# Kernel optimization log

Measured on AMD Instinct MI355X. Metric: run time of the kernel, lower is better.

Reference implementation:

```python
import jax, jax.numpy as jnp
import numpy as np

B, C_IN, H, W = 64, 2048, 14, 14
D, FF, G, NC, NH = 768, 2048, 100, 9605, 8
DF = int(NC / G + 0.999)  # 97
HD = D // NH
EPS = 1e-5


def _ln(x, g, b):
    m = jnp.mean(x, axis=-1, keepdims=True)
    v = jnp.mean(jnp.square(x - m), axis=-1, keepdims=True)
    return (x - m) * jax.lax.rsqrt(v + EPS) * g + b


def setup_inputs() -> dict:
    key = jax.random.key(0)
    ks = jax.random.split(key, 16)
    def xav(k, shape):
        fan_in, fan_out = shape[-1], shape[-2] if len(shape) > 1 else shape[-1]
        std = float(np.sqrt(2.0 / (fan_in + fan_out)))
        return jax.random.normal(k, shape, jnp.float32) * std
    return {
        "x": jax.random.normal(ks[0], (B, C_IN, H, W), jnp.float32),
        "w_embed": xav(ks[1], (D, C_IN)), "b_embed": jnp.zeros((D,), jnp.float32),
        "query_embed": jax.random.normal(ks[2], (G, D), jnp.float32),
        "wq": xav(ks[3], (D, D)), "bq": jnp.zeros((D,), jnp.float32),
        "wk": xav(ks[4], (D, D)), "bk": jnp.zeros((D,), jnp.float32),
        "wv": xav(ks[5], (D, D)), "bv": jnp.zeros((D,), jnp.float32),
        "wo": xav(ks[6], (D, D)), "bo": jnp.zeros((D,), jnp.float32),
        "g1": jnp.ones((D,), jnp.float32), "be1": jnp.zeros((D,), jnp.float32),
        "g2": jnp.ones((D,), jnp.float32), "be2": jnp.zeros((D,), jnp.float32),
        "g3": jnp.ones((D,), jnp.float32), "be3": jnp.zeros((D,), jnp.float32),
        "w1": xav(ks[7], (FF, D)), "bl1": jnp.zeros((FF,), jnp.float32),
        "w2": xav(ks[8], (D, FF)), "bl2": jnp.zeros((D,), jnp.float32),
        "dup_pool": xav(ks[9], (G, D, DF)),
        "dup_bias": jnp.zeros((NC,), jnp.float32),
    }


def reference(x, w_embed, b_embed, query_embed, wq, bq, wk, bk, wv, bv, wo, bo,
              g1, be1, g2, be2, g3, be3, w1, bl1, w2, bl2, dup_pool, dup_bias):
    bs = x.shape[0]
    # [B, C, H, W] -> [B, S, C]
    mem = x.reshape(bs, x.shape[1], -1).transpose(0, 2, 1)
    # embed_standart + relu -> [B, S, D]
    mem = jax.nn.relu(jnp.einsum('bsc,dc->bsd', mem, w_embed) + b_embed)
    # tgt = queries broadcast to batch: [B, G, D]
    tgt = jnp.broadcast_to(query_embed[None], (bs, G, D))
    # layer: tgt = norm1(tgt + dropout1(tgt)) = norm1(2*tgt)
    tgt = _ln(tgt + tgt, g1, be1)
    # cross multihead attention (q=tgt, k=v=mem)
    q = (jnp.einsum('bgd,ed->bge', tgt, wq) + bq).reshape(bs, G, NH, HD)
    k = (jnp.einsum('bsd,ed->bse', mem, wk) + bk).reshape(bs, -1, NH, HD)
    v = (jnp.einsum('bsd,ed->bse', mem, wv) + bv).reshape(bs, -1, NH, HD)
    scores = jnp.einsum('bghd,bshd->bhgs', q, k) / jnp.sqrt(jnp.float32(HD))
    attn = jax.nn.softmax(scores, axis=-1)
    ctx = jnp.einsum('bhgs,bshd->bghd', attn, v).reshape(bs, G, D)
    ctx = jnp.einsum('bgd,ed->bge', ctx, wo) + bo
    tgt = _ln(tgt + ctx, g2, be2)
    # FFN
    ff = jax.nn.relu(jnp.einsum('bgd,fd->bgf', tgt, w1) + bl1)
    ff = jnp.einsum('bgf,df->bgd', ff, w2) + bl2
    h = _ln(tgt + ff, g3, be3)  # [B, G, D]
    # grouped FC: per-group matmul fused into one batched einsum
    out_extrap = jnp.einsum('bgd,gdf->bgf', h, dup_pool)  # [B, G, DF]
    logits = out_extrap.reshape(bs, G * DF)[:, :NC] + dup_bias
    return logits
```

## Files before the change

kernel.cpp:

```cpp
#include <hip/hip_runtime.h>
#include <hip/hip_bf16.h>


#define B_    64
#define CIN_  2048
#define S_    196
#define D_    768
#define FF_   2048
#define G_    100
#define NC_   9605
#define NH_   8
#define HD_   96
#define DF_   97
#define FP_   112
#define GP_   112
#define SP_   224
#define BS_   (B_ * S_)
#define BG_   (B_ * G_)

typedef __bf16 bf16x8 __attribute__((ext_vector_type(8)));
typedef float  f32x4  __attribute__((ext_vector_type(4)));
typedef ushort us8    __attribute__((ext_vector_type(8)));

__device__ __forceinline__ float bf2f(ushort u) {
  union { unsigned int i; float f; } v; v.i = ((unsigned int)u) << 16; return v.f;
}
__device__ __forceinline__ ushort f2bf(float f) {
  __hip_bfloat16 h = __float2bfloat16(f);
  return *reinterpret_cast<ushort*>(&h);
}

__device__ __forceinline__ void gl2lds16(const ushort* g, ushort* l) {
  __builtin_amdgcn_global_load_lds((const __attribute__((address_space(1))) unsigned int*)g,
                                   (__attribute__((address_space(3))) unsigned int*)l, 16, 0, 0);
}

#define XP_BLKS  4096
#define CVP_BLKS 256
#define TG_BLKS  128

struct PrepArgs {
  const float* x;   ushort* aemb;
  const float* csrc[2]; ushort* cdst[2]; int cn4[2]; int ctotal;
  const float* qe; const float* g1; const float* be1;
  float* tgt; ushort* tgtB;
};

__global__ __launch_bounds__(256) void k_prep(PrepArgs pa) {
  __shared__ __align__(16) char smem[196 * 40 * 2];
  int jid = blockIdx.x;
  const int t = threadIdx.x;

  if (jid < XP_BLKS) {
    ushort* xs = (ushort*)smem;
    const int b = jid >> 6, cbase = (jid & 63) * 32;
    const float* xb = pa.x + ((size_t)b * CIN_ + cbase) * S_;
    #pragma unroll
    for (int it = 0; it < 2; ++it) {
      const int u = it * 256 + t;
      if (u < 392) {
        const int j = u >> 3, cq = u & 7;
        const int s = 4 * j;
        float4 a[4];
        #pragma unroll
        for (int r = 0; r < 4; ++r)
          a[r] = *(const float4*)(xb + (size_t)(cq * 4 + r) * S_ + s);
        #pragma unroll
        for (int r = 0; r < 4; ++r) {
          ushort4 o;
          o.x = f2bf(((const float*)&a[0])[r]);
          o.y = f2bf(((const float*)&a[1])[r]);
          o.z = f2bf(((const float*)&a[2])[r]);
          o.w = f2bf(((const float*)&a[3])[r]);
          *(ushort4*)&xs[(s + r) * 40 + cq * 4] = o;
        }
      }
    }
    __syncthreads();
    const int sl = t >> 2, oct = t & 3;
    #pragma unroll
    for (int sr = 0; sr < 4; ++sr) {
      const int s = sr * 64 + sl;
      if (s < S_) {
        us8 v = *(const us8*)&xs[s * 40 + oct * 8];
        *(us8*)&pa.aemb[((size_t)(b * S_ + s)) * CIN_ + cbase + oct * 8] = v;
      }
    }
    return;
  }
  jid -= XP_BLKS;

  if (jid < CVP_BLKS) {
    int i = jid * 256 + t;
    const int stride = CVP_BLKS * 256;
    for (; i < pa.ctotal; i += stride) {
      int seg = 0, off = i;
      while (off >= pa.cn4[seg]) { off -= pa.cn4[seg]; ++seg; }
      const float4* sp = (const float4*)pa.csrc[seg];
      float4 v0 = sp[2 * off], v1 = sp[2 * off + 1];
      us8 o;
      o[0] = f2bf(v0.x); o[1] = f2bf(v0.y); o[2] = f2bf(v0.z); o[3] = f2bf(v0.w);
      o[4] = f2bf(v1.x); o[5] = f2bf(v1.y); o[6] = f2bf(v1.z); o[7] = f2bf(v1.w);
      ((us8*)pa.cdst[seg])[off] = o;
    }
    return;
  }
  jid -= CVP_BLKS;

  float* r1 = (float*)smem;
  float* r2 = r1 + 256;
  const int g = jid;
  if (g >= G_) {
    for (int d = t; d < D_; d += 256) pa.tgtB[(size_t)g * D_ + d] = 0;
    return;
  }
  float y[3]; float s = 0.f, sq = 0.f;
  const float* row = pa.qe + (size_t)g * D_;
  #pragma unroll
  for (int i = 0; i < 3; ++i) { float v = 2.f * row[t + i * 256]; y[i] = v; s += v; sq += v * v; }
  r1[t] = s; r2[t] = sq; __syncthreads();
  for (int o = 128; o > 0; o >>= 1) { if (t < o) { r1[t] += r1[t + o]; r2[t] += r2[t + o]; } __syncthreads(); }
  const float mean = r1[0] * (1.f / D_);
  const float var  = r2[0] * (1.f / D_) - mean * mean;
  const float w = rsqrtf(var + 1e-5f);
  #pragma unroll
  for (int i = 0; i < 3; ++i) {
    int d = t + i * 256;
    float v = (y[i] - mean) * w * pa.g1[d] + pa.be1[d];
    pa.tgt[(size_t)g * D_ + d] = v;
    pa.tgtB[(size_t)g * D_ + d] = f2bf(v);
  }
}

__device__ __forceinline__ void gemm_core(const ushort* __restrict__ A, const ushort* __restrict__ B,
    const float* __restrict__ bias, const float* __restrict__ bias2,
    float* __restrict__ Cf, ushort* __restrict__ Cb, ushort* __restrict__ Vt,
    int N, int K, int m0, int n0, int relu, ushort* As, ushort* Bs) {
  const int t = threadIdx.x;
  const int lane = t & 63, wave = t >> 6;
  const int quad = lane >> 4, lrow = lane & 15;
  const int wr = (wave >> 1) * 64, wc = (wave & 1) * 64;
  const int srow = t >> 2, scol = (t & 3) * 8;
  const ushort* ag = A + (size_t)(m0 + srow) * K + scol;
  const ushort* bg = B + (size_t)(n0 + srow) * K + scol;
  ushort* asw = As + t * 8;
  ushort* bsw = Bs + t * 8;
  f32x4 acc[4][4] = {};
  gl2lds16(ag,                  asw);
  gl2lds16(ag + (size_t)64 * K, asw + 64 * 32);
  gl2lds16(bg,                  bsw);
  gl2lds16(bg + (size_t)64 * K, bsw + 64 * 32);
  int cur = 0;
  for (int k0 = 0; k0 < K; k0 += 32) {
    if (k0 + 32 < K) {
      const int nb = (cur ^ 1) * (128 * 32);
      gl2lds16(ag + k0 + 32,                  asw + nb);
      gl2lds16(ag + k0 + 32 + (size_t)64 * K, asw + nb + 64 * 32);
      gl2lds16(bg + k0 + 32,                  bsw + nb);
      gl2lds16(bg + k0 + 32 + (size_t)64 * K, bsw + nb + 64 * 32);
      asm volatile("s_waitcnt vmcnt(4)" ::: "memory");
    } else {
      asm volatile("s_waitcnt vmcnt(0)" ::: "memory");
    }
    __builtin_amdgcn_s_barrier();
    __builtin_amdgcn_sched_barrier(0);
    const ushort* as = As + cur * (128 * 32);
    const ushort* bs = Bs + cur * (128 * 32);
    bf16x8 af[4], bfr[4];
    #pragma unroll
    for (int i = 0; i < 4; ++i) af[i] = *(const bf16x8*)&as[(wr + i * 16 + lrow) * 32 + quad * 8];
    #pragma unroll
    for (int j = 0; j < 4; ++j) bfr[j] = *(const bf16x8*)&bs[(wc + j * 16 + lrow) * 32 + quad * 8];
    __builtin_amdgcn_s_setprio(1);
    #pragma unroll
    for (int i = 0; i < 4; ++i)
      #pragma unroll
      for (int j = 0; j < 4; ++j)
        acc[i][j] = __builtin_amdgcn_mfma_f32_16x16x32_bf16(af[i], bfr[j], acc[i][j], 0, 0, 0);
    __builtin_amdgcn_s_setprio(0);
    __builtin_amdgcn_sched_barrier(0);
    __builtin_amdgcn_s_barrier();
    __builtin_amdgcn_sched_barrier(0);
    cur ^= 1;
  }
  #pragma unroll
  for (int i = 0; i < 4; ++i) {
    #pragma unroll
    for (int j = 0; j < 4; ++j) {
      const int gcol = n0 + wc + j * 16 + lrow;
      const float bv = (bias2 && gcol >= D_) ? bias2[gcol - D_] : (bias ? bias[gcol] : 0.f);
      if (Vt && gcol >= D_) {
        const int dv = gcol - D_, hh = dv / HD_, hd = dv % HD_;
        const int row0 = m0 + wr + i * 16 + quad * 4;
        const int bb = row0 / S_, ss = row0 % S_;
        ushort4 o;
        o.x = f2bf(acc[i][j][0] + bv);
        o.y = f2bf(acc[i][j][1] + bv);
        o.z = f2bf(acc[i][j][2] + bv);
        o.w = f2bf(acc[i][j][3] + bv);
        *(ushort4*)&Vt[((size_t)(bb * NH_ + hh) * HD_ + hd) * SP_ + ss] = o;
      } else {
        #pragma unroll
        for (int r = 0; r < 4; ++r) {
          const int grow = m0 + wr + i * 16 + quad * 4 + r;
          float v = acc[i][j][r] + bv;
          if (relu) v = fmaxf(v, 0.f);
          if (Cf) Cf[(size_t)grow * N + gcol] = v;
          else    Cb[(size_t)grow * N + gcol] = f2bf(v);
        }
      }
    }
  }
}

__global__ __launch_bounds__(256) void k_gemm(const ushort* __restrict__ A, const ushort* __restrict__ B,
    const float* __restrict__ bias, const float* __restrict__ bias2,
    float* __restrict__ Cf, ushort* __restrict__ Cb, ushort* __restrict__ Vt,
    int N, int K, int nbx, int nm, int relu) {
  __shared__ ushort As[2 * 128 * 32];
  __shared__ ushort Bs[2 * 128 * 32];
  const int l = blockIdx.x;
  const int mb = (l >> 3) / nbx * 8 + (l & 7);
  const int nb = (l >> 3) % nbx;
  if (mb >= nm) return;
  gemm_core(A, B, bias, bias2, Cf, Cb, Vt, N, K, mb * 128, nb * 128, relu, As, Bs);
}
static inline int swz_grid(int nm, int nbx) { return ((nm + 7) & ~7) * nbx; }

__device__ __forceinline__ void gemm_core64(const ushort* __restrict__ A, const ushort* __restrict__ B,
    const float* __restrict__ bias, ushort* __restrict__ Cb,
    int N, int K, int m0, int n0, int relu, ushort* As, ushort* Bs) {
  const int t = threadIdx.x;
  const int lane = t & 63, wave = t >> 6;
  const int quad = lane >> 4, lrow = lane & 15;
  const int wr = (wave >> 1) * 32, wc = (wave & 1) * 64;
  const int srow = t >> 2, scol = (t & 3) * 8;
  const ushort* ag = A + (size_t)(m0 + srow) * K + scol;
  const ushort* bg = B + (size_t)(n0 + srow) * K + scol;
  ushort* asw = As + t * 8;
  ushort* bsw = Bs + t * 8;
  f32x4 acc[2][4] = {};
  gl2lds16(ag,                  asw);
  gl2lds16(bg,                  bsw);
  gl2lds16(bg + (size_t)64 * K, bsw + 64 * 32);
  int cur = 0;
  for (int k0 = 0; k0 < K; k0 += 32) {
    if (k0 + 32 < K) {
      gl2lds16(ag + k0 + 32,                  asw + (cur ^ 1) * (64 * 32));
      gl2lds16(bg + k0 + 32,                  bsw + (cur ^ 1) * (128 * 32));
      gl2lds16(bg + k0 + 32 + (size_t)64 * K, bsw + (cur ^ 1) * (128 * 32) + 64 * 32);
      asm volatile("s_waitcnt vmcnt(3)" ::: "memory");
    } else {
      asm volatile("s_waitcnt vmcnt(0)" ::: "memory");
    }
    __builtin_amdgcn_s_barrier();
    __builtin_amdgcn_sched_barrier(0);
    const ushort* as = As + cur * (64 * 32);
    const ushort* bs = Bs + cur * (128 * 32);
    bf16x8 af[2], bfr[4];
    #pragma unroll
    for (int i = 0; i < 2; ++i) af[i] = *(const bf16x8*)&as[(wr + i * 16 + lrow) * 32 + quad * 8];
    #pragma unroll
    for (int j = 0; j < 4; ++j) bfr[j] = *(const bf16x8*)&bs[(wc + j * 16 + lrow) * 32 + quad * 8];
    __builtin_amdgcn_s_setprio(1);
    #pragma unroll
    for (int i = 0; i < 2; ++i)
      #pragma unroll
      for (int j = 0; j < 4; ++j)
        acc[i][j] = __builtin_amdgcn_mfma_f32_16x16x32_bf16(af[i], bfr[j], acc[i][j], 0, 0, 0);
    __builtin_amdgcn_s_setprio(0);
    __builtin_amdgcn_sched_barrier(0);
    __builtin_amdgcn_s_barrier();
    __builtin_amdgcn_sched_barrier(0);
    cur ^= 1;
  }
  #pragma unroll
  for (int i = 0; i < 2; ++i) {
    #pragma unroll
    for (int j = 0; j < 4; ++j) {
      const int gcol = n0 + wc + j * 16 + lrow;
      const float bv = bias ? bias[gcol] : 0.f;
      #pragma unroll
      for (int r = 0; r < 4; ++r) {
        const int grow = m0 + wr + i * 16 + quad * 4 + r;
        float v = acc[i][j][r] + bv;
        if (relu) v = fmaxf(v, 0.f);
        Cb[(size_t)grow * N + gcol] = f2bf(v);
      }
    }
  }
}

__global__ __launch_bounds__(256) void k_gemm64(const ushort* __restrict__ A, const ushort* __restrict__ B,
    const float* __restrict__ bias, ushort* __restrict__ Cb,
    int N, int K, int nbx, int nm, int relu) {
  __shared__ ushort As[2 * 64 * 32];
  __shared__ ushort Bs[2 * 128 * 32];
  const int l = blockIdx.x;
  const int mb = (l >> 3) / nbx * 8 + (l & 7);
  const int nb = (l >> 3) % nbx;
  if (mb >= nm) return;
  gemm_core64(A, B, bias, Cb, N, K, mb * 64, nb * 128, relu, As, Bs);
}

#define DT2_BLKS 400
#define EG_BLKS  1200
#define QP_BLKS  12
#define CV2_BLKS 256

struct EmbArgs {
  const ushort* aemb; const ushort* wembB; const float* b_embed; ushort* memB;
  const ushort* tgtB; const ushort* wqB;   const float* bq;      ushort* qB;
  const float* dup; ushort* dupT;
  const float* csrc[5]; ushort* cdst[5]; int cn4[5]; int ctotal;
};

__global__ __launch_bounds__(256) void k_embed(EmbArgs ea) {
  __shared__ ushort As[2 * 64 * 32];
  __shared__ ushort Bs[2 * 128 * 32];
  int l = blockIdx.x;
  const int t = threadIdx.x;

  if (l < DT2_BLKS) {
    float (*tile)[33] = (float (*)[33])As;
    const int g = l >> 2, dchunk = l & 3;
    const int tx = t & 31, ty = t >> 5;
    for (int di = 0; di < 6; ++di) {
      const int d0 = dchunk * 192 + di * 32;
      for (int f0 = 0; f0 < 128; f0 += 32) {
        #pragma unroll
        for (int r = 0; r < 32; r += 8) {
          int d = d0 + ty + r, f = f0 + tx;
          tile[ty + r][tx] = (f < DF_) ? ea.dup[(size_t)g * D_ * DF_ + (size_t)d * DF_ + f] : 0.f;
        }
        __syncthreads();
        #pragma unroll
        for (int r = 0; r < 32; r += 8) {
          int f = f0 + ty + r, d = d0 + tx;
          if (f < FP_) ea.dupT[((size_t)g * FP_ + f) * D_ + d] = f2bf(tile[tx][ty + r]);
        }
        __syncthreads();
      }
    }
    return;
  }
  l -= DT2_BLKS;

  if (l < EG_BLKS) {
    const int mb = (l >> 3) / 6 * 8 + (l & 7);
    const int nb = (l >> 3) % 6;
    if (mb >= 196) return;
    gemm_core64(ea.aemb, ea.wembB, ea.b_embed, ea.memB, D_, CIN_, mb * 64, nb * 128, 1, As, Bs);
    return;
  }
  l -= EG_BLKS;

  if (l < QP_BLKS) {
    gemm_core64(ea.tgtB, ea.wqB, ea.bq, ea.qB, D_, D_, (l / 6) * 64, (l % 6) * 128, 0, As, Bs);
    return;
  }
  l -= QP_BLKS;

  int i = l * 256 + t;
  const int stride = CV2_BLKS * 256;
  for (; i < ea.ctotal; i += stride) {
    int seg = 0, off = i;
    while (off >= ea.cn4[seg]) { off -= ea.cn4[seg]; ++seg; }
    const float4* sp = (const float4*)ea.csrc[seg];
    float4 v0 = sp[2 * off], v1 = sp[2 * off + 1];
    us8 o;
    o[0] = f2bf(v0.x); o[1] = f2bf(v0.y); o[2] = f2bf(v0.z); o[3] = f2bf(v0.w);
    o[4] = f2bf(v1.x); o[5] = f2bf(v1.y); o[6] = f2bf(v1.z); o[7] = f2bf(v1.w);
    ((us8*)ea.cdst[seg])[off] = o;
  }
}

__global__ __launch_bounds__(256) void k_attn(const ushort* __restrict__ qB,
    const ushort* __restrict__ Kb, const ushort* __restrict__ VbT, ushort* __restrict__ ctx) {
  __shared__ ushort lds[GP_ * SP_];
  ushort* Ks = lds;
  ushort* Ps = lds;
  const int h = blockIdx.x, b = blockIdx.y, t = threadIdx.x;
  const int bh = b * NH_ + h;
  const int lane = t & 63, wave = t >> 6;
  const int quad = lane >> 4, c = lane & 15;
  for (int i = t; i < 208 * 12; i += 256) {
    int r = i / 12, col = (i % 12) * 8;
    gl2lds16(Kb + ((size_t)(b * S_ + r)) * D_ + h * HD_ + col, &Ks[i * 8]);
  }
  __syncthreads();
  const float scale = 0.1020620726f;
  f32x4 p[2][13];
  #pragma unroll
  for (int rep = 0; rep < 2; ++rep) {
    const int ii = wave + rep * 4;
    if (ii >= 7) continue;
    bf16x8 af[3];
    #pragma unroll
    for (int ks = 0; ks < 3; ++ks)
      af[ks] = *(const bf16x8*)(qB + ((size_t)(ii * 16 + c)) * D_ + h * HD_ + ks * 32 + quad * 8);
    __builtin_amdgcn_s_setprio(1);
    #pragma unroll
    for (int j = 0; j < 13; ++j) {
      f32x4 a = {};
      #pragma unroll
      for (int ks = 0; ks < 3; ++ks) {
        bf16x8 bf = *(const bf16x8*)&Ks[(j * 16 + c) * HD_ + ks * 32 + quad * 8];
        a = __builtin_amdgcn_mfma_f32_16x16x32_bf16(af[ks], bf, a, 0, 0, 0);
      }
      p[rep][j] = a;
    }
    __builtin_amdgcn_s_setprio(0);
    float m[4] = {-1e30f, -1e30f, -1e30f, -1e30f};
    #pragma unroll
    for (int j = 0; j < 13; ++j)
      #pragma unroll
      for (int r = 0; r < 4; ++r) {
        float v = p[rep][j][r] * scale;
        if (j == 12 && c >= 4) v = -1e30f;
        p[rep][j][r] = v;
        m[r] = fmaxf(m[r], v);
      }
    #pragma unroll
    for (int r = 0; r < 4; ++r) {
      m[r] = fmaxf(m[r], __shfl_xor(m[r], 1));
      m[r] = fmaxf(m[r], __shfl_xor(m[r], 2));
      m[r] = fmaxf(m[r], __shfl_xor(m[r], 4));
      m[r] = fmaxf(m[r], __shfl_xor(m[r], 8));
    }
    float lsum[4] = {0.f, 0.f, 0.f, 0.f};
    #pragma unroll
    for (int j = 0; j < 13; ++j)
      #pragma unroll
      for (int r = 0; r < 4; ++r) {
        float e = __expf(p[rep][j][r] - m[r]);
        p[rep][j][r] = e; lsum[r] += e;
      }
    #pragma unroll
    for (int r = 0; r < 4; ++r) {
      lsum[r] += __shfl_xor(lsum[r], 1);
      lsum[r] += __shfl_xor(lsum[r], 2);
      lsum[r] += __shfl_xor(lsum[r], 4);
      lsum[r] += __shfl_xor(lsum[r], 8);
      lsum[r] = 1.f / lsum[r];
    }
    #pragma unroll
    for (int j = 0; j < 13; ++j)
      #pragma unroll
      for (int r = 0; r < 4; ++r)
        p[rep][j][r] *= lsum[r];
  }
  __syncthreads();
  #pragma unroll
  for (int rep = 0; rep < 2; ++rep) {
    const int ii = wave + rep * 4;
    if (ii >= 7) continue;
    #pragma unroll
    for (int r = 0; r < 4; ++r) {
      const int g = ii * 16 + quad * 4 + r;
      #pragma unroll
      for (int j = 0; j < 13; ++j)
        Ps[g * SP_ + j * 16 + c] = f2bf(p[rep][j][r]);
      Ps[g * SP_ + 208 + c] = 0;
    }
  }
  __syncthreads();
  #pragma unroll
  for (int rep = 0; rep < 2; ++rep) {
    const int ii = wave + rep * 4;
    if (ii >= 7) continue;
    bf16x8 af[7];
    #pragma unroll
    for (int k = 0; k < 7; ++k)
      af[k] = *(const bf16x8*)&Ps[(ii * 16 + c) * SP_ + k * 32 + quad * 8];
    #pragma unroll
    for (int j = 0; j < 6; ++j) {
      f32x4 acc = {};
      __builtin_amdgcn_s_setprio(1);
      #pragma unroll
      for (int k = 0; k < 7; ++k) {
        bf16x8 bf = *(const bf16x8*)(VbT + ((size_t)bh * HD_ + j * 16 + c) * SP_ + k * 32 + quad * 8);
        acc = __builtin_amdgcn_mfma_f32_16x16x32_bf16(af[k], bf, acc, 0, 0, 0);
      }
      __builtin_amdgcn_s_setprio(0);
      #pragma unroll
      for (int r = 0; r < 4; ++r) {
        const int g = ii * 16 + quad * 4 + r;
        if (g < G_)
          ctx[((size_t)(b * G_ + g)) * D_ + h * HD_ + j * 16 + c] = f2bf(acc[r]);
      }
    }
  }
}

__global__ __launch_bounds__(256) void k_lnres(const float* __restrict__ resid, int resid_mod,
    const ushort* __restrict__ addB, const float* __restrict__ gamma, const float* __restrict__ beta,
    float* __restrict__ outf, ushort* __restrict__ outb, int transb) {
  const int row = blockIdx.x, t = threadIdx.x;
  __shared__ float r1[256], r2[256];
  const float* rrow = resid + (size_t)(resid_mod ? (row % G_) : row) * D_;
  const ushort* arow = addB + (size_t)row * D_;
  float y[3]; float s = 0.f, sq = 0.f;
  #pragma unroll
  for (int i = 0; i < 3; ++i) {
    int d = t + i * 256;
    float v = rrow[d] + bf2f(arow[d]);
    y[i] = v; s += v; sq += v * v;
  }
  r1[t] = s; r2[t] = sq; __syncthreads();
  for (int o = 128; o > 0; o >>= 1) { if (t < o) { r1[t] += r1[t + o]; r2[t] += r2[t + o]; } __syncthreads(); }
  const float mean = r1[0] * (1.f / D_);
  const float var  = r2[0] * (1.f / D_) - mean * mean;
  const float w = rsqrtf(var + 1e-5f);
  const size_t orow = transb ? ((size_t)(row % G_) * B_ + row / G_) : (size_t)row;
  #pragma unroll
  for (int i = 0; i < 3; ++i) {
    int d = t + i * 256;
    float v = (y[i] - mean) * w * gamma[d] + beta[d];
    if (outf) outf[(size_t)row * D_ + d] = v;
    if (outb) outb[orow * D_ + d] = f2bf(v);
  }
}

__global__ __launch_bounds__(256) void k_head4(const ushort* __restrict__ hT,
    const ushort* __restrict__ dupT, const float* __restrict__ dup_bias, float* __restrict__ out) {
  const int g = blockIdx.x, j = blockIdx.y, t = threadIdx.x;
  const int lane = t & 63, wave = t >> 6;
  const int quad = lane >> 4, c = lane & 15;
  const ushort* ap = hT + ((size_t)g * B_ + wave * 16 + c) * D_;
  const ushort* bp = dupT + ((size_t)g * FP_ + j * 16 + c) * D_;
  f32x4 acc = {};
  #pragma unroll 8
  for (int k0 = 0; k0 < D_; k0 += 32) {
    bf16x8 af = *(const bf16x8*)(ap + k0 + quad * 8);
    bf16x8 bf = *(const bf16x8*)(bp + k0 + quad * 8);
    acc = __builtin_amdgcn_mfma_f32_16x16x32_bf16(af, bf, acc, 0, 0, 0);
  }
  const int f = j * 16 + c;
  if (f >= DF_) return;
  const int n = g * DF_ + f;
  if (n >= NC_) return;
  const float bv = dup_bias[n];
  #pragma unroll
  for (int r = 0; r < 4; ++r) {
    const int b = wave * 16 + quad * 4 + r;
    out[(size_t)b * NC_ + n] = acc[r] + bv;
  }
}

static constexpr size_t OFF_AEMB  = 0;
static constexpr size_t OFF_VBT   = 0;
static constexpr size_t OFF_FF    = 0;
static constexpr size_t OFF_FFO   = 26214400;
static constexpr size_t OFF_WEMB  = 51380224;
static constexpr size_t OFF_MEM   = 54525952;
static constexpr size_t OFF_WK    = 73793536;
static constexpr size_t OFF_WV    = 74973184;
static constexpr size_t OFF_WO    = 76152832;
static constexpr size_t OFF_W1    = 77332480;
static constexpr size_t OFF_W2    = 80478208;
static constexpr size_t OFF_DUP   = 83623936;
static constexpr size_t OFF_KB    = 100827136;
static constexpr size_t OFF_TGT   = 139362304;
static constexpr size_t OFF_TGTB  = 139669504;
static constexpr size_t OFF_Q     = 139866112;
static constexpr size_t OFF_CTX   = 140068864;
static constexpr size_t OFF_WQ    = OFF_CTX;
static constexpr size_t OFF_CTXO  = 149899264;
static constexpr size_t OFF_TGT2F = 169560064;
static constexpr size_t OFF_TGT2B = 189220864;
static constexpr size_t OFF_HB    = 199051264;

extern "C" void kernel_launch(void* const* d_in, const int* in_sizes, int n_in,
                              void* d_out, int out_size, void* d_ws, size_t ws_size,
                              hipStream_t stream) {
  const float* x           = (const float*)d_in[0];
  const float* w_embed     = (const float*)d_in[1];
  const float* b_embed     = (const float*)d_in[2];
  const float* query_embed = (const float*)d_in[3];
  const float* wq          = (const float*)d_in[4];
  const float* bq          = (const float*)d_in[5];
  const float* wk          = (const float*)d_in[6];
  const float* bk          = (const float*)d_in[7];
  const float* wv          = (const float*)d_in[8];
  const float* bv          = (const float*)d_in[9];
  const float* wo          = (const float*)d_in[10];
  const float* bo          = (const float*)d_in[11];
  const float* g1          = (const float*)d_in[12];
  const float* be1         = (const float*)d_in[13];
  const float* g2          = (const float*)d_in[14];
  const float* be2         = (const float*)d_in[15];
  const float* g3          = (const float*)d_in[16];
  const float* be3         = (const float*)d_in[17];
  const float* w1          = (const float*)d_in[18];
  const float* bl1         = (const float*)d_in[19];
  const float* w2          = (const float*)d_in[20];
  const float* bl2         = (const float*)d_in[21];
  const float* dup_pool    = (const float*)d_in[22];
  const float* dup_bias    = (const float*)d_in[23];
  float* out = (float*)d_out;
  char* ws = (char*)d_ws;

  ushort* aemb  = (ushort*)(ws + OFF_AEMB);
  ushort* wembB = (ushort*)(ws + OFF_WEMB);
  ushort* memB  = (ushort*)(ws + OFF_MEM);
  ushort* wkvB  = (ushort*)(ws + OFF_WK);
  ushort* wkB   = (ushort*)(ws + OFF_WK);
  ushort* wvB   = (ushort*)(ws + OFF_WV);
  ushort* woB   = (ushort*)(ws + OFF_WO);
  ushort* w1B   = (ushort*)(ws + OFF_W1);
  ushort* w2B   = (ushort*)(ws + OFF_W2);
  ushort* wqB   = (ushort*)(ws + OFF_WQ);
  ushort* dupT  = (ushort*)(ws + OFF_DUP);
  ushort* Kb    = (ushort*)(ws + OFF_KB);
  float*  tgtF  = (float*)(ws + OFF_TGT);
  ushort* tgtB  = (ushort*)(ws + OFF_TGTB);
  ushort* qB    = (ushort*)(ws + OFF_Q);
  ushort* VbT   = (ushort*)(ws + OFF_VBT);
  ushort* ctxB  = (ushort*)(ws + OFF_CTX);
  ushort* ctxoB = (ushort*)(ws + OFF_CTXO);
  float*  tgt2F = (float*)(ws + OFF_TGT2F);
  ushort* tgt2B = (ushort*)(ws + OFF_TGT2B);
  ushort* ffB   = (ushort*)(ws + OFF_FF);
  ushort* ffoB  = (ushort*)(ws + OFF_FFO);
  ushort* hT    = (ushort*)(ws + OFF_HB);

  PrepArgs pa;
  pa.x = x; pa.aemb = aemb;
  pa.csrc[0] = w_embed; pa.cdst[0] = wembB; pa.cn4[0] = D_ * CIN_ / 8;
  pa.csrc[1] = wq;      pa.cdst[1] = wqB;   pa.cn4[1] = D_ * D_ / 8;
  pa.ctotal = pa.cn4[0] + pa.cn4[1];
  pa.qe = query_embed; pa.g1 = g1; pa.be1 = be1; pa.tgt = tgtF; pa.tgtB = tgtB;
  k_prep<<<XP_BLKS + CVP_BLKS + TG_BLKS, 256, 0, stream>>>(pa);

  EmbArgs ea;
  ea.aemb = aemb; ea.wembB = wembB; ea.b_embed = b_embed; ea.memB = memB;
  ea.tgtB = tgtB; ea.wqB = wqB; ea.bq = bq; ea.qB = qB;
  ea.dup = dup_pool; ea.dupT = dupT;
  ea.csrc[0] = wk; ea.cdst[0] = wkB; ea.cn4[0] = D_ * D_ / 8;
  ea.csrc[1] = wv; ea.cdst[1] = wvB; ea.cn4[1] = D_ * D_ / 8;
  ea.csrc[2] = wo; ea.cdst[2] = woB; ea.cn4[2] = D_ * D_ / 8;
  ea.csrc[3] = w1; ea.cdst[3] = w1B; ea.cn4[3] = FF_ * D_ / 8;
  ea.csrc[4] = w2; ea.cdst[4] = w2B; ea.cn4[4] = D_ * FF_ / 8;
  ea.ctotal = ea.cn4[0] + ea.cn4[1] + ea.cn4[2] + ea.cn4[3] + ea.cn4[4];
  k_embed<<<DT2_BLKS + EG_BLKS + QP_BLKS + CV2_BLKS, 256, 0, stream>>>(ea);

  k_gemm<<<swz_grid(98, 12), 256, 0, stream>>>(memB, wkvB, bk, bv, nullptr, Kb, VbT,
                                               D_, D_, 12, 98, 0);

  k_attn<<<dim3(NH_, B_), 256, 0, stream>>>(qB, Kb, VbT, ctxB);

  k_gemm64<<<swz_grid(100, 6), 256, 0, stream>>>(ctxB, woB, bo, ctxoB, D_, D_, 6, 100, 0);

  k_lnres<<<BG_, 256, 0, stream>>>(tgtF, 1, ctxoB, g2, be2, tgt2F, tgt2B, 0);

  k_gemm<<<swz_grid(50, 16), 256, 0, stream>>>(tgt2B, w1B, bl1, nullptr, nullptr, ffB, nullptr,
                                               FF_, D_, 16, 50, 1);
  k_gemm64<<<swz_grid(100, 6), 256, 0, stream>>>(ffB, w2B, bl2, ffoB, D_, FF_, 6, 100, 0);

  k_lnres<<<BG_, 256, 0, stream>>>(tgt2F, 0, ffoB, g3, be3, nullptr, hT, 1);

  k_head4<<<dim3(G_, 7), 256, 0, stream>>>(hT, dupT, dup_bias, out);
}
```

Before: 556.6 us.

## Fuse input transpose and bf16 conversion into embedding GEMM A-tile loads

Removes the separate pass that transposed the fp32 NCHW input into a bf16 [B*S, C] buffer. The embedding GEMM now reads fp32 x directly, converts and transposes it into LDS per K-step, and loads B through global-to-LDS copies from half of the threads. This drops the write and re-read of a 51MB intermediate. In exchange, the new GEMM core loses double buffering and does A conversion inline with strided fp32 reads, with every A tile re-read by each of the 6 N-blocks.

```diff
diff --git a/kernel.cpp b/kernel.cpp
--- a/kernel.cpp
+++ b/kernel.cpp
@@ -35,60 +35,19 @@
                                    (__attribute__((address_space(3))) unsigned int*)l, 16, 0, 0);
 }
 
-#define XP_BLKS  4096
-#define CVP_BLKS 256
+#define CVP_BLKS 1024
 #define TG_BLKS  128
 
 struct PrepArgs {
-  const float* x;   ushort* aemb;
   const float* csrc[2]; ushort* cdst[2]; int cn4[2]; int ctotal;
   const float* qe; const float* g1; const float* be1;
   float* tgt; ushort* tgtB;
 };
 
 __global__ __launch_bounds__(256) void k_prep(PrepArgs pa) {
-  __shared__ __align__(16) char smem[196 * 40 * 2];
+  __shared__ float r1[256], r2[256];
   int jid = blockIdx.x;
   const int t = threadIdx.x;
-
-  if (jid < XP_BLKS) {
-    ushort* xs = (ushort*)smem;
-    const int b = jid >> 6, cbase = (jid & 63) * 32;
-    const float* xb = pa.x + ((size_t)b * CIN_ + cbase) * S_;
-    #pragma unroll
-    for (int it = 0; it < 2; ++it) {
-      const int u = it * 256 + t;
-      if (u < 392) {
-        const int j = u >> 3, cq = u & 7;
-        const int s = 4 * j;
-        float4 a[4];
-        #pragma unroll
-        for (int r = 0; r < 4; ++r)
-          a[r] = *(const float4*)(xb + (size_t)(cq * 4 + r) * S_ + s);
-        #pragma unroll
-        for (int r = 0; r < 4; ++r) {
-          ushort4 o;
-          o.x = f2bf(((const float*)&a[0])[r]);
-          o.y = f2bf(((const float*)&a[1])[r]);
-          o.z = f2bf(((const float*)&a[2])[r]);
-          o.w = f2bf(((const float*)&a[3])[r]);
-          *(ushort4*)&xs[(s + r) * 40 + cq * 4] = o;
-        }
-      }
-    }
-    __syncthreads();
-    const int sl = t >> 2, oct = t & 3;
-    #pragma unroll
-    for (int sr = 0; sr < 4; ++sr) {
-      const int s = sr * 64 + sl;
-      if (s < S_) {
-        us8 v = *(const us8*)&xs[s * 40 + oct * 8];
-        *(us8*)&pa.aemb[((size_t)(b * S_ + s)) * CIN_ + cbase + oct * 8] = v;
-      }
-    }
-    return;
-  }
-  jid -= XP_BLKS;
 
   if (jid < CVP_BLKS) {
     int i = jid * 256 + t;
@@ -107,8 +66,6 @@
   }
   jid -= CVP_BLKS;
 
-  float* r1 = (float*)smem;
-  float* r2 = r1 + 256;
   const int g = jid;
   if (g >= G_) {
     for (int d = t; d < D_; d += 256) pa.tgtB[(size_t)g * D_ + d] = 0;
@@ -303,13 +260,79 @@
   gemm_core64(A, B, bias, Cb, N, K, mb * 64, nb * 128, relu, As, Bs);
 }
 
+__device__ __forceinline__ void gemm_core64_xa(const float* __restrict__ X,
+    const ushort* __restrict__ Bw, const float* __restrict__ bias, ushort* __restrict__ Cb,
+    int m0, int n0, ushort* As, ushort* Bs) {
+  const int t = threadIdx.x;
+  const int lane = t & 63, wave = t >> 6;
+  const int quad = lane >> 4, lrow = lane & 15;
+  const int wr = (wave >> 1) * 32, wc = (wave & 1) * 64;
+  f32x4 acc[2][4] = {};
+  const int j = t & 15, q = t >> 4;
+  const int arow = m0 + 4 * j;
+  const float* px = X + ((size_t)(arow / S_) * CIN_) * S_ + (arow % S_);
+  const int tb = t - 128;
+  const ushort* bg = Bw + (size_t)(n0 + (tb >> 2)) * CIN_ + (tb & 3) * 8;
+  ushort* bsw = Bs + tb * 8;
+  for (int k0 = 0; k0 < CIN_; k0 += 32) {
+    if (t < 128) {
+      const float* pc = px + (size_t)(k0 + 4 * q) * S_;
+      float4 a0 = *(const float4*)(pc);
+      float4 a1 = *(const float4*)(pc + S_);
+      float4 a2 = *(const float4*)(pc + 2 * S_);
+      float4 a3 = *(const float4*)(pc + 3 * S_);
+      ushort4 o0 = { f2bf(a0.x), f2bf(a1.x), f2bf(a2.x), f2bf(a3.x) };
+      ushort4 o1 = { f2bf(a0.y), f2bf(a1.y), f2bf(a2.y), f2bf(a3.y) };
+      ushort4 o2 = { f2bf(a0.z), f2bf(a1.z), f2bf(a2.z), f2bf(a3.z) };
+      ushort4 o3 = { f2bf(a0.w), f2bf(a1.w), f2bf(a2.w), f2bf(a3.w) };
+      *(ushort4*)&As[(4 * j + 0) * 32 + 4 * q] = o0;
+      *(ushort4*)&As[(4 * j + 1) * 32 + 4 * q] = o1;
+      *(ushort4*)&As[(4 * j + 2) * 32 + 4 * q] = o2;
+      *(ushort4*)&As[(4 * j + 3) * 32 + 4 * q] = o3;
+    } else {
+      gl2lds16(bg + k0,                       bsw);
+      gl2lds16(bg + k0 + (size_t)32 * CIN_,   bsw + 32 * 32);
+      gl2lds16(bg + k0 + (size_t)64 * CIN_,   bsw + 64 * 32);
+      gl2lds16(bg + k0 + (size_t)96 * CIN_,   bsw + 96 * 32);
+    }
+    __syncthreads();
+    bf16x8 af[2], bfr[4];
+    #pragma unroll
+    for (int i = 0; i < 2; ++i) af[i] = *(const bf16x8*)&As[(wr + i * 16 + lrow) * 32 + quad * 8];
+    #pragma unroll
+    for (int jj = 0; jj < 4; ++jj) bfr[jj] = *(const bf16x8*)&Bs[(wc + jj * 16 + lrow) * 32 + quad * 8];
+    __builtin_amdgcn_s_setprio(1);
+    #pragma unroll
+    for (int i = 0; i < 2; ++i)
+      #pragma unroll
+      for (int jj = 0; jj < 4; ++jj)
+        acc[i][jj] = __builtin_amdgcn_mfma_f32_16x16x32_bf16(af[i], bfr[jj], acc[i][jj], 0, 0, 0);
+    __builtin_amdgcn_s_setprio(0);
+    __syncthreads();
+  }
+  #pragma unroll
+  for (int i = 0; i < 2; ++i) {
+    #pragma unroll
+    for (int jj = 0; jj < 4; ++jj) {
+      const int gcol = n0 + wc + jj * 16 + lrow;
+      const float bv = bias[gcol];
+      #pragma unroll
+      for (int r = 0; r < 4; ++r) {
+        const int grow = m0 + wr + i * 16 + quad * 4 + r;
+        float v = fmaxf(acc[i][jj][r] + bv, 0.f);
+        Cb[(size_t)grow * D_ + gcol] = f2bf(v);
+      }
+    }
+  }
+}
+
 #define DT2_BLKS 400
 #define EG_BLKS  1200
 #define QP_BLKS  12
 #define CV2_BLKS 256
 
 struct EmbArgs {
-  const ushort* aemb; const ushort* wembB; const float* b_embed; ushort* memB;
+  const float* x; const ushort* wembB; const float* b_embed; ushort* memB;
   const ushort* tgtB; const ushort* wqB;   const float* bq;      ushort* qB;
   const float* dup; ushort* dupT;
   const float* csrc[5]; ushort* cdst[5]; int cn4[5]; int ctotal;
@@ -350,7 +373,7 @@
     const int mb = (l >> 3) / 6 * 8 + (l & 7);
     const int nb = (l >> 3) % 6;
     if (mb >= 196) return;
-    gemm_core64(ea.aemb, ea.wembB, ea.b_embed, ea.memB, D_, CIN_, mb * 64, nb * 128, 1, As, Bs);
+    gemm_core64_xa(ea.x, ea.wembB, ea.b_embed, ea.memB, mb * 64, nb * 128, As, Bs);
     return;
   }
   l -= EG_BLKS;
@@ -548,7 +571,6 @@
   }
 }
 
-static constexpr size_t OFF_AEMB  = 0;
 static constexpr size_t OFF_VBT   = 0;
 static constexpr size_t OFF_FF    = 0;
 static constexpr size_t OFF_FFO   = 26214400;
@@ -601,7 +623,6 @@
   float* out = (float*)d_out;
   char* ws = (char*)d_ws;
 
-  ushort* aemb  = (ushort*)(ws + OFF_AEMB);
   ushort* wembB = (ushort*)(ws + OFF_WEMB);
   ushort* memB  = (ushort*)(ws + OFF_MEM);
   ushort* wkvB  = (ushort*)(ws + OFF_WK);
@@ -626,15 +647,14 @@
   ushort* hT    = (ushort*)(ws + OFF_HB);
 
   PrepArgs pa;
-  pa.x = x; pa.aemb = aemb;
   pa.csrc[0] = w_embed; pa.cdst[0] = wembB; pa.cn4[0] = D_ * CIN_ / 8;
   pa.csrc[1] = wq;      pa.cdst[1] = wqB;   pa.cn4[1] = D_ * D_ / 8;
   pa.ctotal = pa.cn4[0] + pa.cn4[1];
   pa.qe = query_embed; pa.g1 = g1; pa.be1 = be1; pa.tgt = tgtF; pa.tgtB = tgtB;
-  k_prep<<<XP_BLKS + CVP_BLKS + TG_BLKS, 256, 0, stream>>>(pa);
+  k_prep<<<CVP_BLKS + TG_BLKS, 256, 0, stream>>>(pa);
 
   EmbArgs ea;
-  ea.aemb = aemb; ea.wembB = wembB; ea.b_embed = b_embed; ea.memB = memB;
+  ea.x = x; ea.wembB = wembB; ea.b_embed = b_embed; ea.memB = memB;
   ea.tgtB = tgtB; ea.wqB = wqB; ea.bq = bq; ea.qB = qB;
   ea.dup = dup_pool; ea.dupT = dupT;
   ea.csrc[0] = wk; ea.cdst[0] = wkB; ea.cn4[0] = D_ * D_ / 8;
```

Result: slower. 599.1 us (+7.6%).
